# Performance work log

Measured on AMD Instinct MI355X. Metric: run time of the kernel, lower is better.

## Reference

```python
import jax, jax.numpy as jnp
import numpy as np

N_NODES = 40000
N_EDGES = 640000
IN_C = 128
HID = 32
HEADS = 4
OUT_C = 8
NUM_GRAPHS = 64
NEG_SLOPE = 0.2


def setup_inputs() -> dict:
    key = jax.random.key(0)
    ks = jax.random.split(key, 16)
    x = jax.random.normal(ks[0], (N_NODES, IN_C), dtype=jnp.float32)
    edge_index = jax.random.randint(ks[1], (2, N_EDGES), 0, N_NODES, dtype=jnp.int64)
    batch = jnp.sort(jax.random.randint(ks[2], (N_NODES,), 0, NUM_GRAPHS, dtype=jnp.int64))
    s = lambda k, shape, fan_in: jax.random.normal(k, shape, jnp.float32) / np.sqrt(fan_in)
    # conv0: in -> hid, 4 heads, concat
    W0 = s(ks[3], (IN_C, HEADS * HID), IN_C)
    a_src0 = s(ks[4], (HEADS, HID), HID)
    a_dst0 = s(ks[5], (HEADS, HID), HID)
    b0 = jnp.zeros((HEADS * HID,), jnp.float32)
    # conv1: hid*H -> hid, 4 heads, concat
    W1 = s(ks[6], (HEADS * HID, HEADS * HID), HEADS * HID)
    a_src1 = s(ks[7], (HEADS, HID), HID)
    a_dst1 = s(ks[8], (HEADS, HID), HID)
    b1 = jnp.zeros((HEADS * HID,), jnp.float32)
    # conv2: hid*H -> hid, 1 head, no concat
    W2 = s(ks[9], (HEADS * HID, HID), HEADS * HID)
    a_src2 = s(ks[10], (1, HID), HID)
    a_dst2 = s(ks[11], (1, HID), HID)
    b2 = jnp.zeros((HID,), jnp.float32)
    lin1_w = s(ks[12], (HID, IN_C), HID)
    lin1_b = jnp.zeros((IN_C,), jnp.float32)
    lin2_w = s(ks[13], (IN_C, OUT_C), IN_C)
    lin2_b = jnp.zeros((OUT_C,), jnp.float32)
    return dict(x=x, edge_index=edge_index, batch=batch,
                W0=W0, a_src0=a_src0, a_dst0=a_dst0, b0=b0,
                W1=W1, a_src1=a_src1, a_dst1=a_dst1, b1=b1,
                W2=W2, a_src2=a_src2, a_dst2=a_dst2, b2=b2,
                lin1_w=lin1_w, lin1_b=lin1_b, lin2_w=lin2_w, lin2_b=lin2_b)


def gat_conv(x, src, dst, W, a_src, a_dst, b, heads, out_c, concat):
    N = x.shape[0]
    h = (x @ W).reshape(N, heads, out_c)          # [N,H,C]
    als = (h * a_src[None]).sum(-1)               # [N,H]
    ald = (h * a_dst[None]).sum(-1)               # [N,H]
    e = jax.nn.leaky_relu(als[src] + ald[dst], NEG_SLOPE)  # [E,H]
    m = jax.ops.segment_max(e, dst, num_segments=N)
    m = jnp.where(jnp.isfinite(m), m, 0.0)
    p = jnp.exp(e - m[dst])                       # [E,H]
    denom = jax.ops.segment_sum(p, dst, num_segments=N)
    alpha = p / jnp.maximum(denom[dst], 1e-16)
    out = jax.ops.segment_sum(h[src] * alpha[:, :, None], dst, num_segments=N)
    out = out.reshape(N, heads * out_c) if concat else out.mean(axis=1)
    return out + b


def reference(x, edge_index, batch,
              W0, a_src0, a_dst0, b0,
              W1, a_src1, a_dst1, b1,
              W2, a_src2, a_dst2, b2,
              lin1_w, lin1_b, lin2_w, lin2_b):
    N = x.shape[0]
    # PyG GATConv adds self-loops by default
    loop = jnp.arange(N, dtype=edge_index.dtype)
    src = jnp.concatenate([edge_index[0], loop])
    dst = jnp.concatenate([edge_index[1], loop])
    # eval mode: dropout is identity
    h = jax.nn.elu(gat_conv(x, src, dst, W0, a_src0, a_dst0, b0, HEADS, HID, True))
    h = jax.nn.elu(gat_conv(h, src, dst, W1, a_src1, a_dst1, b1, HEADS, HID, True))
    h = jax.nn.elu(gat_conv(h, src, dst, W2, a_src2, a_dst2, b2, 1, HID, False))
    # global mean pool over graphs
    sums = jax.ops.segment_sum(h, batch, num_segments=NUM_GRAPHS)
    cnts = jax.ops.segment_sum(jnp.ones((N, 1), h.dtype), batch, num_segments=NUM_GRAPHS)
    g = sums / jnp.maximum(cnts, 1.0)             # [G, HID]
    g = jax.nn.relu(g @ lin1_w + lin1_b)
    return g @ lin2_w + lin2_b                    # [G, OUT_C]
```

## Files before the change

kernel.cpp:

```cpp
#include <hip/hip_runtime.h>
#include <hip/hip_bf16.h>

#define N_NODES 40000
#define N_EDGES 640000
#define E_TOT   (N_EDGES + N_NODES)
#define NUM_GRAPHS 64
#define CAP_SHIFT 6

#define CVTX_BLOCKS 5000
#define CVTW_BLOCKS 144
#define CVT_BLOCKS (CVTX_BLOCKS + CVTW_BLOCKS)
#define EBLOCKS ((E_TOT + 255) / 256)
#define GEMM_BLOCKS 625

typedef __attribute__((ext_vector_type(8))) short bf16x8;
typedef __attribute__((ext_vector_type(4))) float f32x4;

__device__ inline float bf2f(unsigned short u) {
    union { unsigned int i; float f; } v; v.i = ((unsigned int)u) << 16; return v.f;
}
__device__ inline unsigned short f2bf(float f) {
    union { float f; unsigned int i; } v; v.f = f;
    unsigned int r = v.i + 0x7FFF + ((v.i >> 16) & 1);
    return (unsigned short)(r >> 16);
}


__global__ __launch_bounds__(256) void cvt_kernel(const float* __restrict__ x,
                                                  const float* __restrict__ W0,
                                                  const float* __restrict__ W1,
                                                  const float* __restrict__ W2,
                                                  unsigned short* __restrict__ Xb,
                                                  unsigned short* __restrict__ Wt0,
                                                  unsigned short* __restrict__ Wt1,
                                                  unsigned short* __restrict__ Wt2) {
    int b = blockIdx.x;
    int tid = threadIdx.x;
    if (b < CVTX_BLOCKS) {
        int i = b * 256 + tid;
        float4 v = ((const float4*)x)[i];
        ushort4 o;
        o.x = f2bf(v.x); o.y = f2bf(v.y); o.z = f2bf(v.z); o.w = f2bf(v.w);
        ((ushort4*)Xb)[i] = o;
    } else {
        int idx = (b - CVTX_BLOCKS) * 256 + tid;
        if (idx < 16384) {
            int n = idx >> 7, k = idx & 127;
            Wt0[idx] = f2bf(W0[k * 128 + n]);
        } else if (idx < 32768) {
            int i = idx - 16384;
            int n = i >> 7, k = i & 127;
            Wt1[i] = f2bf(W1[k * 128 + n]);
        } else if (idx < 36864) {
            int i = idx - 32768;
            int n = i >> 7, k = i & 127;
            Wt2[i] = f2bf(W2[k * 32 + n]);
        }
    }
}


__device__ __forceinline__ void gemm128_body(int blk,
                                             const unsigned short* __restrict__ Xb,
                                             const unsigned short* __restrict__ Wt,
                                             const float* __restrict__ asrc,
                                             const float* __restrict__ adst,
                                             unsigned short* __restrict__ Hb,
                                             float* __restrict__ ALS_t,
                                             float* __restrict__ ALD_t) {
    int wave = threadIdx.x >> 6;
    int lane = threadIdx.x & 63;
    int l15 = lane & 15;
    int q = lane >> 4;
    int r0 = (blk * 4 + wave) * 16;

    f32x4 acc[8];
#pragma unroll
    for (int t = 0; t < 8; ++t) acc[t] = (f32x4){0.f, 0.f, 0.f, 0.f};

    float asv[8], adv[8];
#pragma unroll
    for (int t = 0; t < 8; ++t) {
        int c = t * 16 + l15;
        asv[t] = asrc[c];
        adv[t] = adst[c];
    }

    const unsigned short* xrow = Xb + (long)(r0 + l15) * 128 + q * 8;
    const unsigned short* wrow = Wt + (long)l15 * 128 + q * 8;
#pragma unroll
    for (int kt = 0; kt < 4; ++kt) {
        bf16x8 a = *(const bf16x8*)(xrow + kt * 32);
#pragma unroll
        for (int t = 0; t < 8; ++t) {
            bf16x8 b = *(const bf16x8*)(wrow + (long)t * 16 * 128 + kt * 32);
            acc[t] = __builtin_amdgcn_mfma_f32_16x16x32_bf16(a, b, acc[t], 0, 0, 0);
        }
    }

#pragma unroll
    for (int t = 0; t < 8; ++t)
#pragma unroll
        for (int i = 0; i < 4; ++i)
            Hb[(long)(r0 + q * 4 + i) * 128 + t * 16 + l15] = f2bf(acc[t][i]);

#pragma unroll
    for (int i = 0; i < 4; ++i) {
        float ps0 = acc[0][i] * asv[0] + acc[1][i] * asv[1];
        float ps1 = acc[2][i] * asv[2] + acc[3][i] * asv[3];
        float ps2 = acc[4][i] * asv[4] + acc[5][i] * asv[5];
        float ps3 = acc[6][i] * asv[6] + acc[7][i] * asv[7];
        float pd0 = acc[0][i] * adv[0] + acc[1][i] * adv[1];
        float pd1 = acc[2][i] * adv[2] + acc[3][i] * adv[3];
        float pd2 = acc[4][i] * adv[4] + acc[5][i] * adv[5];
        float pd3 = acc[6][i] * adv[6] + acc[7][i] * adv[7];
#pragma unroll
        for (int m = 1; m < 16; m <<= 1) {
            ps0 += __shfl_xor(ps0, m, 16); ps1 += __shfl_xor(ps1, m, 16);
            ps2 += __shfl_xor(ps2, m, 16); ps3 += __shfl_xor(ps3, m, 16);
            pd0 += __shfl_xor(pd0, m, 16); pd1 += __shfl_xor(pd1, m, 16);
            pd2 += __shfl_xor(pd2, m, 16); pd3 += __shfl_xor(pd3, m, 16);
        }
        int r = r0 + q * 4 + i;
        if (l15 < 4) {
            float v = (l15 == 0) ? ps0 : (l15 == 1) ? ps1 : (l15 == 2) ? ps2 : ps3;
            ALS_t[l15 * N_NODES + r] = v;
        } else if (l15 < 8) {
            int h = l15 - 4;
            float v = (h == 0) ? pd0 : (h == 1) ? pd1 : (h == 2) ? pd2 : pd3;
            ALD_t[h * N_NODES + r] = v;
        }
    }
}


__global__ __launch_bounds__(256) void gemm_scatter_kernel(const unsigned short* __restrict__ Xb,
                                                           const unsigned short* __restrict__ Wt,
                                                           const float* __restrict__ asrc,
                                                           const float* __restrict__ adst,
                                                           unsigned short* __restrict__ Hb,
                                                           float* __restrict__ ALS_t,
                                                           float* __restrict__ ALD_t,
                                                           const int* __restrict__ esrc,
                                                           const int* __restrict__ edst,
                                                           int* __restrict__ cnt,
                                                           int* __restrict__ psrc) {
    int b = blockIdx.x;
    if (b < GEMM_BLOCKS) {
        gemm128_body(b, Xb, Wt, asrc, adst, Hb, ALS_t, ALD_t);
    } else {
        int e = (b - GEMM_BLOCKS) * 256 + threadIdx.x;
        if (e < E_TOT) {
            int d, s;
            if (e < N_EDGES) { d = edst[e]; s = esrc[e]; }
            else             { d = e - N_EDGES; s = d; }
            int slot = atomicAdd(&cnt[d], 1);
            psrc[(d << CAP_SHIFT) + slot] = s;
        }
    }
}

__global__ __launch_bounds__(256) void gemm128_mfma(const unsigned short* __restrict__ Xb,
                                                    const unsigned short* __restrict__ Wt,
                                                    const float* __restrict__ asrc,
                                                    const float* __restrict__ adst,
                                                    unsigned short* __restrict__ Hb,
                                                    float* __restrict__ ALS_t,
                                                    float* __restrict__ ALD_t) {
    gemm128_body(blockIdx.x, Xb, Wt, asrc, adst, Hb, ALS_t, ALD_t);
}

__global__ __launch_bounds__(256) void gemm32_mfma(const unsigned short* __restrict__ Xb,
                                                   const unsigned short* __restrict__ Wt2,
                                                   const float* __restrict__ asrc,
                                                   const float* __restrict__ adst,
                                                   unsigned short* __restrict__ H2b,
                                                   float* __restrict__ ALS,
                                                   float* __restrict__ ALD) {
    int wave = threadIdx.x >> 6;
    int lane = threadIdx.x & 63;
    int l15 = lane & 15;
    int q = lane >> 4;
    int r0 = (blockIdx.x * 4 + wave) * 16;

    f32x4 acc[2];
    acc[0] = (f32x4){0.f, 0.f, 0.f, 0.f};
    acc[1] = (f32x4){0.f, 0.f, 0.f, 0.f};

    const unsigned short* xrow = Xb + (long)(r0 + l15) * 128 + q * 8;
    const unsigned short* wrow = Wt2 + (long)l15 * 128 + q * 8;
#pragma unroll
    for (int kt = 0; kt < 4; ++kt) {
        bf16x8 a = *(const bf16x8*)(xrow + kt * 32);
#pragma unroll
        for (int t = 0; t < 2; ++t) {
            bf16x8 b = *(const bf16x8*)(wrow + (long)t * 16 * 128 + kt * 32);
            acc[t] = __builtin_amdgcn_mfma_f32_16x16x32_bf16(a, b, acc[t], 0, 0, 0);
        }
    }

    float as0 = asrc[l15], as1 = asrc[16 + l15];
    float ad0 = adst[l15], ad1 = adst[16 + l15];
#pragma unroll
    for (int t = 0; t < 2; ++t)
#pragma unroll
        for (int i = 0; i < 4; ++i)
            H2b[(long)(r0 + q * 4 + i) * 32 + t * 16 + l15] = f2bf(acc[t][i]);

#pragma unroll
    for (int i = 0; i < 4; ++i) {
        float ps = acc[0][i] * as0 + acc[1][i] * as1;
        float pd = acc[0][i] * ad0 + acc[1][i] * ad1;
#pragma unroll
        for (int m = 1; m < 16; m <<= 1) {
            ps += __shfl_xor(ps, m, 16);
            pd += __shfl_xor(pd, m, 16);
        }
        if (l15 == 0) {
            int r = r0 + q * 4 + i;
            ALS[r] = ps;
            ALD[r] = pd;
        }
    }
}

__global__ __launch_bounds__(256) void agg128(const unsigned short* __restrict__ Hb,
                                              const float* __restrict__ ALS_t,
                                              const float* __restrict__ ALD_t,
                                              const int* __restrict__ cnt,
                                              const int* __restrict__ psrc,
                                              const float* __restrict__ bias,
                                              unsigned short* __restrict__ OUTb) {
    int n = blockIdx.x * 4 + (threadIdx.x >> 6);
    n = __builtin_amdgcn_readfirstlane(n);
    if (n >= N_NODES) return;
    int lane = threadIdx.x & 63;
    int c = lane * 2;
    int head = lane >> 4;
    int e16 = lane & 15;
    float aldh = ALD_t[head * N_NODES + n];
    const float* alsh = ALS_t + (long)head * N_NODES;
    int j0 = n << CAP_SHIFT;
    int j1 = j0 + __builtin_amdgcn_readfirstlane(cnt[n]);
    float a0 = 0.f, a1 = 0.f, dsum = 0.f;
    for (int jb = j0; jb < j1; jb += 16) {
        int j = jb + e16;
        int jc = (j < j1) ? j : (j1 - 1);
        int s = psrc[jc];
        float e = alsh[s] + aldh;
        e = (e > 0.f) ? e : 0.2f * e;
        float w = (j < j1) ? __expf(e) : 0.f;
        int st[16]; float wt[16];
#pragma unroll
        for (int t = 0; t < 16; ++t) {
            st[t] = __shfl(s, t, 16);
            wt[t] = __shfl(w, t, 16);
        }
        unsigned int hv[16];
#pragma unroll
        for (int t = 0; t < 16; ++t)
            hv[t] = *(const unsigned int*)(Hb + (long)st[t] * 128 + c);
#pragma unroll
        for (int t = 0; t < 16; ++t) {
            float h0 = bf2f((unsigned short)(hv[t] & 0xFFFF));
            float h1 = bf2f((unsigned short)(hv[t] >> 16));
            dsum += wt[t];
            a0 += wt[t] * h0;
            a1 += wt[t] * h1;
        }
    }
    float inv = 1.0f / dsum;
    float o0 = a0 * inv + bias[c];
    float o1 = a1 * inv + bias[c + 1];
    o0 = (o0 > 0.f) ? o0 : (__expf(o0) - 1.f);
    o1 = (o1 > 0.f) ? o1 : (__expf(o1) - 1.f);
    ushort2 ob; ob.x = f2bf(o0); ob.y = f2bf(o1);
    *(ushort2*)(OUTb + (long)n * 128 + c) = ob;
}

__global__ __launch_bounds__(256) void agg32(const unsigned short* __restrict__ H2b,
                                             const float* __restrict__ ALS,
                                             const float* __restrict__ ALD,
                                             const int* __restrict__ cnt,
                                             const int* __restrict__ psrc,
                                             const float* __restrict__ bias,
                                             float* __restrict__ OUT) {
    int wv = blockIdx.x * 4 + (threadIdx.x >> 6);
    int lane = threadIdx.x & 63;
    int col = lane & 31;
    int half = lane >> 5;
    int e16 = lane & 15;
    int n = wv * 2 + half;
    if (n >= N_NODES) return;
    float aldn = ALD[n];
    int j0 = n << CAP_SHIFT;
    int j1 = j0 + cnt[n];
    float a = 0.f, dsum = 0.f;
    for (int jb = j0; jb < j1; jb += 16) {
        int j = jb + e16;
        int jc = (j < j1) ? j : (j1 - 1);
        int s = psrc[jc];
        float e = ALS[s] + aldn;
        e = (e > 0.f) ? e : 0.2f * e;
        float w = (j < j1) ? __expf(e) : 0.f;
        int st[16]; float wt[16];
#pragma unroll
        for (int t = 0; t < 16; ++t) {
            st[t] = __shfl(s, t, 16);
            wt[t] = __shfl(w, t, 16);
        }
        unsigned short hv[16];
#pragma unroll
        for (int t = 0; t < 16; ++t)
            hv[t] = H2b[st[t] * 32 + col];
#pragma unroll
        for (int t = 0; t < 16; ++t) {
            dsum += wt[t];
            a += wt[t] * bf2f(hv[t]);
        }
    }
    float o = a / dsum + bias[col];
    o = (o > 0.f) ? o : (__expf(o) - 1.f);
    OUT[n * 32 + col] = o;
}

__global__ __launch_bounds__(256) void pool_kernel(const float* __restrict__ H3,
                                                   const int* __restrict__ batch,
                                                   float* __restrict__ gsum,
                                                   float* __restrict__ gcnt) {
    const int CHUNK = 40;
    int gid = (blockIdx.x * 256 + threadIdx.x) >> 5;
    int c = threadIdx.x & 31;
    int n0 = gid * CHUNK;
    if (n0 >= N_NODES) return;
    int n1 = n0 + CHUNK;
    if (n1 > N_NODES) n1 = N_NODES;
    int cur = batch[n0];
    float acc = 0.f;
    int cnt = 0;
    for (int n = n0; n < n1; ++n) {
        int b = batch[n];
        if (b != cur) {
            atomicAdd(&gsum[cur * 32 + c], acc);
            if (c == 0) atomicAdd(&gcnt[cur], (float)cnt);
            cur = b; acc = 0.f; cnt = 0;
        }
        acc += H3[n * 32 + c];
        cnt++;
    }
    atomicAdd(&gsum[cur * 32 + c], acc);
    if (c == 0) atomicAdd(&gcnt[cur], (float)cnt);
}

__global__ __launch_bounds__(256) void mlp_kernel(const float* __restrict__ gsum,
                                                  const float* __restrict__ gcnt,
                                                  const float* __restrict__ l1w,
                                                  const float* __restrict__ l1b,
                                                  const float* __restrict__ l2w,
                                                  const float* __restrict__ l2b,
                                                  float* __restrict__ out) {
    __shared__ float g[NUM_GRAPHS * 32];
    __shared__ float t1[NUM_GRAPHS * 128];
    int tid = threadIdx.x;
    for (int i = tid; i < NUM_GRAPHS * 32; i += 256) {
        float c = gcnt[i >> 5];
        g[i] = gsum[i] / fmaxf(c, 1.0f);
    }
    __syncthreads();
    for (int i = tid; i < NUM_GRAPHS * 128; i += 256) {
        int r = i >> 7, j = i & 127;
        float a = l1b[j];
        for (int k = 0; k < 32; ++k) a += g[r * 32 + k] * l1w[k * 128 + j];
        t1[i] = fmaxf(a, 0.f);
    }
    __syncthreads();
    for (int i = tid; i < NUM_GRAPHS * 8; i += 256) {
        int r = i >> 3, j = i & 7;
        float a = l2b[j];
        for (int k = 0; k < 128; ++k) a += t1[r * 128 + k] * l2w[k * 8 + j];
        out[i] = a;
    }
}


extern "C" void kernel_launch(void* const* d_in, const int* in_sizes, int n_in,
                              void* d_out, int out_size, void* d_ws, size_t ws_size,
                              hipStream_t stream) {
    const float* x      = (const float*)d_in[0];
    const int*   eidx   = (const int*)d_in[1];
    const int*   batch  = (const int*)d_in[2];
    const float* W0     = (const float*)d_in[3];
    const float* asrc0  = (const float*)d_in[4];
    const float* adst0  = (const float*)d_in[5];
    const float* b0     = (const float*)d_in[6];
    const float* W1     = (const float*)d_in[7];
    const float* asrc1  = (const float*)d_in[8];
    const float* adst1  = (const float*)d_in[9];
    const float* b1     = (const float*)d_in[10];
    const float* W2     = (const float*)d_in[11];
    const float* asrc2  = (const float*)d_in[12];
    const float* adst2  = (const float*)d_in[13];
    const float* b2     = (const float*)d_in[14];
    const float* l1w    = (const float*)d_in[15];
    const float* l1b    = (const float*)d_in[16];
    const float* l2w    = (const float*)d_in[17];
    const float* l2b    = (const float*)d_in[18];
    float* out = (float*)d_out;

    const int* esrc = eidx;
    const int* edst = eidx + N_EDGES;

    float* ALS  = (float*)d_ws;
    float* ALD  = ALS + N_NODES * 4;
    float* h3   = ALD + N_NODES * 4;
    int* cnt    = (int*)(h3 + (long)N_NODES * 32);
    float* gsum = (float*)(cnt + N_NODES);
    float* gcnt = gsum + NUM_GRAPHS * 32;
    int* psrc   = (int*)(gcnt + NUM_GRAPHS);
    uintptr_t p = (uintptr_t)(psrc + ((long)N_NODES << CAP_SHIFT));
    p = (p + 15) & ~(uintptr_t)15;
    unsigned short* Xb   = (unsigned short*)p;
    unsigned short* Hb   = Xb + (long)N_NODES * 128;
    unsigned short* OUTb = Hb + (long)N_NODES * 128;
    unsigned short* H2b  = OUTb + (long)N_NODES * 128;
    unsigned short* Wt0  = H2b + (long)N_NODES * 32;
    unsigned short* Wt1  = Wt0 + 128 * 128;
    unsigned short* Wt2  = Wt1 + 128 * 128;

    size_t zbytes = (size_t)(N_NODES + NUM_GRAPHS * 32 + NUM_GRAPHS) * 4;
    hipMemsetAsync(cnt, 0, zbytes, stream);

    cvt_kernel<<<CVT_BLOCKS, 256, 0, stream>>>(x, W0, W1, W2, Xb, Wt0, Wt1, Wt2);

    gemm_scatter_kernel<<<GEMM_BLOCKS + EBLOCKS, 256, 0, stream>>>(
        Xb, Wt0, asrc0, adst0, Hb, ALS, ALD, esrc, edst, cnt, psrc);
    agg128<<<10000, 256, 0, stream>>>(Hb, ALS, ALD, cnt, psrc, b0, OUTb);

    gemm128_mfma<<<GEMM_BLOCKS, 256, 0, stream>>>(OUTb, Wt1, asrc1, adst1, Hb, ALS, ALD);
    agg128<<<10000, 256, 0, stream>>>(Hb, ALS, ALD, cnt, psrc, b1, OUTb);

    gemm32_mfma<<<GEMM_BLOCKS, 256, 0, stream>>>(OUTb, Wt2, asrc2, adst2, H2b, ALS, ALD);
    agg32<<<5000, 256, 0, stream>>>(H2b, ALS, ALD, cnt, psrc, b2, h3);

    pool_kernel<<<125, 256, 0, stream>>>(h3, batch, gsum, gcnt);
    mlp_kernel<<<1, 256, 0, stream>>>(gsum, gcnt, l1w, l1b, l2w, l2b, out);
}
```

Baseline: 294.0 us.

## Compress edge lists to 16-bit, interleave attention logits, trim aggregation tails

The CSR source list is stored as 16-bit indices, written with nontemporal stores, which halves its footprint; node ids stay below 65536 so this is safe. The per-head attention logits move from head-major to node-major [N,4], so each edge gather touches one cache line. Both aggregation kernels skip the unused slots of the last 16-edge chunk using a wave-uniform count. agg32 now gives each wave a single node and splits edges across the two half-waves, combining them with a cross-half shuffle. The cost is a bit more control flow and a hard dependence on the node count fitting in 16 bits.

```diff
diff --git a/kernel.cpp b/kernel.cpp
--- a/kernel.cpp
+++ b/kernel.cpp
@@ -66,8 +66,8 @@
                                              const float* __restrict__ asrc,
                                              const float* __restrict__ adst,
                                              unsigned short* __restrict__ Hb,
-                                             float* __restrict__ ALS_t,
-                                             float* __restrict__ ALD_t) {
+                                             float* __restrict__ ALS4,
+                                             float* __restrict__ ALD4) {
     int wave = threadIdx.x >> 6;
     int lane = threadIdx.x & 63;
     int l15 = lane & 15;
@@ -124,11 +124,11 @@
         int r = r0 + q * 4 + i;
         if (l15 < 4) {
             float v = (l15 == 0) ? ps0 : (l15 == 1) ? ps1 : (l15 == 2) ? ps2 : ps3;
-            ALS_t[l15 * N_NODES + r] = v;
+            ALS4[r * 4 + l15] = v;
         } else if (l15 < 8) {
             int h = l15 - 4;
             float v = (h == 0) ? pd0 : (h == 1) ? pd1 : (h == 2) ? pd2 : pd3;
-            ALD_t[h * N_NODES + r] = v;
+            ALD4[r * 4 + h] = v;
         }
     }
 }
@@ -139,15 +139,15 @@
                                                            const float* __restrict__ asrc,
                                                            const float* __restrict__ adst,
                                                            unsigned short* __restrict__ Hb,
-                                                           float* __restrict__ ALS_t,
-                                                           float* __restrict__ ALD_t,
+                                                           float* __restrict__ ALS4,
+                                                           float* __restrict__ ALD4,
                                                            const int* __restrict__ esrc,
                                                            const int* __restrict__ edst,
                                                            int* __restrict__ cnt,
-                                                           int* __restrict__ psrc) {
+                                                           unsigned short* __restrict__ psrc) {
     int b = blockIdx.x;
     if (b < GEMM_BLOCKS) {
-        gemm128_body(b, Xb, Wt, asrc, adst, Hb, ALS_t, ALD_t);
+        gemm128_body(b, Xb, Wt, asrc, adst, Hb, ALS4, ALD4);
     } else {
         int e = (b - GEMM_BLOCKS) * 256 + threadIdx.x;
         if (e < E_TOT) {
@@ -155,7 +155,8 @@
             if (e < N_EDGES) { d = edst[e]; s = esrc[e]; }
             else             { d = e - N_EDGES; s = d; }
             int slot = atomicAdd(&cnt[d], 1);
-            psrc[(d << CAP_SHIFT) + slot] = s;
+            unsigned short sv = (unsigned short)s;
+            __builtin_nontemporal_store(sv, &psrc[(d << CAP_SHIFT) + slot]);
         }
     }
 }
@@ -165,9 +166,9 @@
                                                     const float* __restrict__ asrc,
                                                     const float* __restrict__ adst,
                                                     unsigned short* __restrict__ Hb,
-                                                    float* __restrict__ ALS_t,
-                                                    float* __restrict__ ALD_t) {
-    gemm128_body(blockIdx.x, Xb, Wt, asrc, adst, Hb, ALS_t, ALD_t);
+                                                    float* __restrict__ ALS4,
+                                                    float* __restrict__ ALD4) {
+    gemm128_body(blockIdx.x, Xb, Wt, asrc, adst, Hb, ALS4, ALD4);
 }
 
 __global__ __launch_bounds__(256) void gemm32_mfma(const unsigned short* __restrict__ Xb,
@@ -225,10 +226,10 @@
 }
 
 __global__ __launch_bounds__(256) void agg128(const unsigned short* __restrict__ Hb,
-                                              const float* __restrict__ ALS_t,
-                                              const float* __restrict__ ALD_t,
+                                              const float* __restrict__ ALS4,
+                                              const float* __restrict__ ALD4,
                                               const int* __restrict__ cnt,
-                                              const int* __restrict__ psrc,
+                                              const unsigned short* __restrict__ psrc,
                                               const float* __restrict__ bias,
                                               unsigned short* __restrict__ OUTb) {
     int n = blockIdx.x * 4 + (threadIdx.x >> 6);
@@ -238,35 +239,38 @@
     int c = lane * 2;
     int head = lane >> 4;
     int e16 = lane & 15;
-    float aldh = ALD_t[head * N_NODES + n];
-    const float* alsh = ALS_t + (long)head * N_NODES;
+    float aldh = ALD4[n * 4 + head];
     int j0 = n << CAP_SHIFT;
-    int j1 = j0 + __builtin_amdgcn_readfirstlane(cnt[n]);
+    int deg = __builtin_amdgcn_readfirstlane(cnt[n]);
+    int j1 = j0 + deg;
     float a0 = 0.f, a1 = 0.f, dsum = 0.f;
     for (int jb = j0; jb < j1; jb += 16) {
+        int tm = j1 - jb; tm = (tm > 16) ? 16 : tm;
         int j = jb + e16;
         int jc = (j < j1) ? j : (j1 - 1);
-        int s = psrc[jc];
-        float e = alsh[s] + aldh;
+        int s = (int)psrc[jc];
+        float e = ALS4[s * 4 + head] + aldh;
         e = (e > 0.f) ? e : 0.2f * e;
         float w = (j < j1) ? __expf(e) : 0.f;
         int st[16]; float wt[16];
+        unsigned int hv[16];
 #pragma unroll
         for (int t = 0; t < 16; ++t) {
-            st[t] = __shfl(s, t, 16);
-            wt[t] = __shfl(w, t, 16);
-        }
-        unsigned int hv[16];
-#pragma unroll
-        for (int t = 0; t < 16; ++t)
-            hv[t] = *(const unsigned int*)(Hb + (long)st[t] * 128 + c);
+            if (t < tm) {
+                st[t] = __shfl(s, t, 16);
+                wt[t] = __shfl(w, t, 16);
+                hv[t] = *(const unsigned int*)(Hb + (long)st[t] * 128 + c);
+            }
+        }
 #pragma unroll
         for (int t = 0; t < 16; ++t) {
-            float h0 = bf2f((unsigned short)(hv[t] & 0xFFFF));
-            float h1 = bf2f((unsigned short)(hv[t] >> 16));
-            dsum += wt[t];
-            a0 += wt[t] * h0;
-            a1 += wt[t] * h1;
+            if (t < tm) {
+                float h0 = bf2f((unsigned short)(hv[t] & 0xFFFF));
+                float h1 = bf2f((unsigned short)(hv[t] >> 16));
+                dsum += wt[t];
+                a0 += wt[t] * h0;
+                a1 += wt[t] * h1;
+            }
         }
     }
     float inv = 1.0f / dsum;
@@ -282,46 +286,54 @@
                                              const float* __restrict__ ALS,
                                              const float* __restrict__ ALD,
                                              const int* __restrict__ cnt,
-                                             const int* __restrict__ psrc,
+                                             const unsigned short* __restrict__ psrc,
                                              const float* __restrict__ bias,
                                              float* __restrict__ OUT) {
-    int wv = blockIdx.x * 4 + (threadIdx.x >> 6);
+    int n = blockIdx.x * 4 + (threadIdx.x >> 6);
+    n = __builtin_amdgcn_readfirstlane(n);
+    if (n >= N_NODES) return;
     int lane = threadIdx.x & 63;
     int col = lane & 31;
-    int half = lane >> 5;
     int e16 = lane & 15;
-    int n = wv * 2 + half;
-    if (n >= N_NODES) return;
+    int chalf = lane >> 5;
     float aldn = ALD[n];
     int j0 = n << CAP_SHIFT;
-    int j1 = j0 + cnt[n];
+    int deg = __builtin_amdgcn_readfirstlane(cnt[n]);
+    int j1 = j0 + deg;
     float a = 0.f, dsum = 0.f;
-    for (int jb = j0; jb < j1; jb += 16) {
-        int j = jb + e16;
+    for (int jb = j0; jb < j1; jb += 32) {
+        int tm = j1 - jb; tm = (tm > 16) ? 16 : tm;
+        int j = jb + chalf * 16 + e16;
         int jc = (j < j1) ? j : (j1 - 1);
-        int s = psrc[jc];
+        int s = (int)psrc[jc];
         float e = ALS[s] + aldn;
         e = (e > 0.f) ? e : 0.2f * e;
         float w = (j < j1) ? __expf(e) : 0.f;
         int st[16]; float wt[16];
+        unsigned short hv[16];
 #pragma unroll
         for (int t = 0; t < 16; ++t) {
-            st[t] = __shfl(s, t, 16);
-            wt[t] = __shfl(w, t, 16);
-        }
-        unsigned short hv[16];
-#pragma unroll
-        for (int t = 0; t < 16; ++t)
-            hv[t] = H2b[st[t] * 32 + col];
+            if (t < tm) {
+                st[t] = __shfl(s, t, 16);
+                wt[t] = __shfl(w, t, 16);
+                hv[t] = H2b[st[t] * 32 + col];
+            }
+        }
 #pragma unroll
         for (int t = 0; t < 16; ++t) {
-            dsum += wt[t];
-            a += wt[t] * bf2f(hv[t]);
-        }
-    }
-    float o = a / dsum + bias[col];
-    o = (o > 0.f) ? o : (__expf(o) - 1.f);
-    OUT[n * 32 + col] = o;
+            if (t < tm) {
+                dsum += wt[t];
+                a += wt[t] * bf2f(hv[t]);
+            }
+        }
+    }
+    a += __shfl_xor(a, 32, 64);
+    dsum += __shfl_xor(dsum, 32, 64);
+    if (chalf == 0) {
+        float o = a / dsum + bias[col];
+        o = (o > 0.f) ? o : (__expf(o) - 1.f);
+        OUT[n * 32 + col] = o;
+    }
 }
 
 __global__ __launch_bounds__(256) void pool_kernel(const float* __restrict__ H3,
@@ -416,7 +428,7 @@
     int* cnt    = (int*)(h3 + (long)N_NODES * 32);
     float* gsum = (float*)(cnt + N_NODES);
     float* gcnt = gsum + NUM_GRAPHS * 32;
-    int* psrc   = (int*)(gcnt + NUM_GRAPHS);
+    unsigned short* psrc = (unsigned short*)(gcnt + NUM_GRAPHS);
     uintptr_t p = (uintptr_t)(psrc + ((long)N_NODES << CAP_SHIFT));
     p = (p + 15) & ~(uintptr_t)15;
     unsigned short* Xb   = (unsigned short*)p;
@@ -440,7 +452,7 @@
     agg128<<<10000, 256, 0, stream>>>(Hb, ALS, ALD, cnt, psrc, b1, OUTb);
 
     gemm32_mfma<<<GEMM_BLOCKS, 256, 0, stream>>>(OUTb, Wt2, asrc2, adst2, H2b, ALS, ALD);
-    agg32<<<5000, 256, 0, stream>>>(H2b, ALS, ALD, cnt, psrc, b2, h3);
+    agg32<<<10000, 256, 0, stream>>>(H2b, ALS, ALD, cnt, psrc, b2, h3);
 
     pool_kernel<<<125, 256, 0, stream>>>(h3, batch, gsum, gcnt);
     mlp_kernel<<<1, 256, 0, stream>>>(gsum, gcnt, l1w, l1b, l2w, l2b, out);
```

Result: slower. 304.2 us (+3.5%).

## Move edge scatter into convert kernel, 16-bit indices, node-major attention logits

Applied to the files above, without the earlier changes.

The CSR-style edge scatter now runs inside the conversion kernel instead of the first GEMM kernel. Its atomics are issued in phases by destination range to improve locality. Source indices are stored as 16-bit values, which halves index traffic in the aggregation kernels; this is only valid while node ids fit in 16 bits, and N=40000 does. Per-head attention logits are now stored node-major ([N,4]) so a gathered source fetches its heads contiguously, in exchange for a simpler GEMM launch.

```diff
diff --git a/kernel.cpp b/kernel.cpp
--- a/kernel.cpp
+++ b/kernel.cpp
@@ -12,6 +12,7 @@
 #define CVT_BLOCKS (CVTX_BLOCKS + CVTW_BLOCKS)
 #define EBLOCKS ((E_TOT + 255) / 256)
 #define GEMM_BLOCKS 625
+#define NPHASE 5
 
 typedef __attribute__((ext_vector_type(8))) short bf16x8;
 typedef __attribute__((ext_vector_type(4))) float f32x4;
@@ -26,14 +27,18 @@
 }
 
 
-__global__ __launch_bounds__(256) void cvt_kernel(const float* __restrict__ x,
-                                                  const float* __restrict__ W0,
-                                                  const float* __restrict__ W1,
-                                                  const float* __restrict__ W2,
-                                                  unsigned short* __restrict__ Xb,
-                                                  unsigned short* __restrict__ Wt0,
-                                                  unsigned short* __restrict__ Wt1,
-                                                  unsigned short* __restrict__ Wt2) {
+__global__ __launch_bounds__(256) void cvt_scatter_kernel(const float* __restrict__ x,
+                                                          const float* __restrict__ W0,
+                                                          const float* __restrict__ W1,
+                                                          const float* __restrict__ W2,
+                                                          unsigned short* __restrict__ Xb,
+                                                          unsigned short* __restrict__ Wt0,
+                                                          unsigned short* __restrict__ Wt1,
+                                                          unsigned short* __restrict__ Wt2,
+                                                          const int* __restrict__ esrc,
+                                                          const int* __restrict__ edst,
+                                                          int* __restrict__ cnt,
+                                                          unsigned short* __restrict__ psrc) {
     int b = blockIdx.x;
     int tid = threadIdx.x;
     if (b < CVTX_BLOCKS) {
@@ -42,7 +47,7 @@
         ushort4 o;
         o.x = f2bf(v.x); o.y = f2bf(v.y); o.z = f2bf(v.z); o.w = f2bf(v.w);
         ((ushort4*)Xb)[i] = o;
-    } else {
+    } else if (b < CVT_BLOCKS) {
         int idx = (b - CVTX_BLOCKS) * 256 + tid;
         if (idx < 16384) {
             int n = idx >> 7, k = idx & 127;
@@ -56,6 +61,20 @@
             int n = i >> 7, k = i & 127;
             Wt2[i] = f2bf(W2[k * 32 + n]);
         }
+    } else {
+        int e = (b - CVT_BLOCKS) * 256 + tid;
+        int d = -1, s = 0;
+        if (e < E_TOT) {
+            if (e < N_EDGES) { d = edst[e]; s = esrc[e]; }
+            else             { d = e - N_EDGES; s = d; }
+        }
+#pragma unroll
+        for (int p = 0; p < NPHASE; ++p) {
+            if (d >= 0 && (d >> 13) == p) {
+                int slot = atomicAdd(&cnt[d], 1);
+                psrc[(d << CAP_SHIFT) + slot] = (unsigned short)s;
+            }
+        }
     }
 }
 
@@ -66,8 +85,8 @@
                                              const float* __restrict__ asrc,
                                              const float* __restrict__ adst,
                                              unsigned short* __restrict__ Hb,
-                                             float* __restrict__ ALS_t,
-                                             float* __restrict__ ALD_t) {
+                                             float* __restrict__ ALS4,
+                                             float* __restrict__ ALD4) {
     int wave = threadIdx.x >> 6;
     int lane = threadIdx.x & 63;
     int l15 = lane & 15;
@@ -124,38 +143,11 @@
         int r = r0 + q * 4 + i;
         if (l15 < 4) {
             float v = (l15 == 0) ? ps0 : (l15 == 1) ? ps1 : (l15 == 2) ? ps2 : ps3;
-            ALS_t[l15 * N_NODES + r] = v;
+            ALS4[r * 4 + l15] = v;
         } else if (l15 < 8) {
             int h = l15 - 4;
             float v = (h == 0) ? pd0 : (h == 1) ? pd1 : (h == 2) ? pd2 : pd3;
-            ALD_t[h * N_NODES + r] = v;
-        }
-    }
-}
-
-
-__global__ __launch_bounds__(256) void gemm_scatter_kernel(const unsigned short* __restrict__ Xb,
-                                                           const unsigned short* __restrict__ Wt,
-                                                           const float* __restrict__ asrc,
-                                                           const float* __restrict__ adst,
-                                                           unsigned short* __restrict__ Hb,
-                                                           float* __restrict__ ALS_t,
-                                                           float* __restrict__ ALD_t,
-                                                           const int* __restrict__ esrc,
-                                                           const int* __restrict__ edst,
-                                                           int* __restrict__ cnt,
-                                                           int* __restrict__ psrc) {
-    int b = blockIdx.x;
-    if (b < GEMM_BLOCKS) {
-        gemm128_body(b, Xb, Wt, asrc, adst, Hb, ALS_t, ALD_t);
-    } else {
-        int e = (b - GEMM_BLOCKS) * 256 + threadIdx.x;
-        if (e < E_TOT) {
-            int d, s;
-            if (e < N_EDGES) { d = edst[e]; s = esrc[e]; }
-            else             { d = e - N_EDGES; s = d; }
-            int slot = atomicAdd(&cnt[d], 1);
-            psrc[(d << CAP_SHIFT) + slot] = s;
+            ALD4[r * 4 + h] = v;
         }
     }
 }
@@ -165,9 +157,9 @@
                                                     const float* __restrict__ asrc,
                                                     const float* __restrict__ adst,
                                                     unsigned short* __restrict__ Hb,
-                                                    float* __restrict__ ALS_t,
-                                                    float* __restrict__ ALD_t) {
-    gemm128_body(blockIdx.x, Xb, Wt, asrc, adst, Hb, ALS_t, ALD_t);
+                                                    float* __restrict__ ALS4,
+                                                    float* __restrict__ ALD4) {
+    gemm128_body(blockIdx.x, Xb, Wt, asrc, adst, Hb, ALS4, ALD4);
 }
 
 __global__ __launch_bounds__(256) void gemm32_mfma(const unsigned short* __restrict__ Xb,
@@ -225,10 +217,10 @@
 }
 
 __global__ __launch_bounds__(256) void agg128(const unsigned short* __restrict__ Hb,
-                                              const float* __restrict__ ALS_t,
-                                              const float* __restrict__ ALD_t,
+                                              const float* __restrict__ ALS4,
+                                              const float* __restrict__ ALD4,
                                               const int* __restrict__ cnt,
-                                              const int* __restrict__ psrc,
+                                              const unsigned short* __restrict__ psrc,
                                               const float* __restrict__ bias,
                                               unsigned short* __restrict__ OUTb) {
     int n = blockIdx.x * 4 + (threadIdx.x >> 6);
@@ -238,16 +230,15 @@
     int c = lane * 2;
     int head = lane >> 4;
     int e16 = lane & 15;
-    float aldh = ALD_t[head * N_NODES + n];
-    const float* alsh = ALS_t + (long)head * N_NODES;
+    float aldh = ALD4[n * 4 + head];
     int j0 = n << CAP_SHIFT;
     int j1 = j0 + __builtin_amdgcn_readfirstlane(cnt[n]);
     float a0 = 0.f, a1 = 0.f, dsum = 0.f;
     for (int jb = j0; jb < j1; jb += 16) {
         int j = jb + e16;
         int jc = (j < j1) ? j : (j1 - 1);
-        int s = psrc[jc];
-        float e = alsh[s] + aldh;
+        int s = (int)psrc[jc];
+        float e = ALS4[s * 4 + head] + aldh;
         e = (e > 0.f) ? e : 0.2f * e;
         float w = (j < j1) ? __expf(e) : 0.f;
         int st[16]; float wt[16];
@@ -282,7 +273,7 @@
                                              const float* __restrict__ ALS,
                                              const float* __restrict__ ALD,
                                              const int* __restrict__ cnt,
-                                             const int* __restrict__ psrc,
+                                             const unsigned short* __restrict__ psrc,
                                              const float* __restrict__ bias,
                                              float* __restrict__ OUT) {
     int wv = blockIdx.x * 4 + (threadIdx.x >> 6);
@@ -299,7 +290,7 @@
     for (int jb = j0; jb < j1; jb += 16) {
         int j = jb + e16;
         int jc = (j < j1) ? j : (j1 - 1);
-        int s = psrc[jc];
+        int s = (int)psrc[jc];
         float e = ALS[s] + aldn;
         e = (e > 0.f) ? e : 0.2f * e;
         float w = (j < j1) ? __expf(e) : 0.f;
@@ -416,7 +407,7 @@
     int* cnt    = (int*)(h3 + (long)N_NODES * 32);
     float* gsum = (float*)(cnt + N_NODES);
     float* gcnt = gsum + NUM_GRAPHS * 32;
-    int* psrc   = (int*)(gcnt + NUM_GRAPHS);
+    unsigned short* psrc = (unsigned short*)(gcnt + NUM_GRAPHS);
     uintptr_t p = (uintptr_t)(psrc + ((long)N_NODES << CAP_SHIFT));
     p = (p + 15) & ~(uintptr_t)15;
     unsigned short* Xb   = (unsigned short*)p;
@@ -430,10 +421,10 @@
     size_t zbytes = (size_t)(N_NODES + NUM_GRAPHS * 32 + NUM_GRAPHS) * 4;
     hipMemsetAsync(cnt, 0, zbytes, stream);
 
-    cvt_kernel<<<CVT_BLOCKS, 256, 0, stream>>>(x, W0, W1, W2, Xb, Wt0, Wt1, Wt2);
-
-    gemm_scatter_kernel<<<GEMM_BLOCKS + EBLOCKS, 256, 0, stream>>>(
-        Xb, Wt0, asrc0, adst0, Hb, ALS, ALD, esrc, edst, cnt, psrc);
+    cvt_scatter_kernel<<<CVT_BLOCKS + EBLOCKS, 256, 0, stream>>>(
+        x, W0, W1, W2, Xb, Wt0, Wt1, Wt2, esrc, edst, cnt, psrc);
+
+    gemm128_mfma<<<GEMM_BLOCKS, 256, 0, stream>>>(Xb, Wt0, asrc0, adst0, Hb, ALS, ALD);
     agg128<<<10000, 256, 0, stream>>>(Hb, ALS, ALD, cnt, psrc, b0, OUTb);
 
     gemm128_mfma<<<GEMM_BLOCKS, 256, 0, stream>>>(OUTb, Wt1, asrc1, adst1, Hb, ALS, ALD);
```

Measured after the change: 294.9 us. No clear change (+0.3%).
